# Kernel tuning notes

Measured on AMD Instinct MI355X. Metric: run time of the kernel, lower is better.

The kernel has to match this reference:

```python
import jax, jax.numpy as jnp
import numpy as np

DIM_IN = 1024
DIM_OUT = 1024
NUM_HEADS = 16
HEAD_DIM = DIM_OUT // NUM_HEADS


def setup_inputs() -> dict:
    key = jax.random.key(0)
    k1, k2, k3, k4 = jax.random.split(key, 4)
    X = jax.random.normal(k1, (4, 2048, DIM_IN), dtype=jnp.float32)
    W_qkv = jax.random.normal(k2, (DIM_IN, 3 * DIM_OUT), dtype=jnp.float32) * (DIM_IN ** -0.5)
    W_out = jax.random.normal(k3, (DIM_OUT, DIM_OUT), dtype=jnp.float32) * (DIM_OUT ** -0.5)
    b_out = jax.random.normal(k4, (DIM_OUT,), dtype=jnp.float32) * 0.01
    return {"X": X, "W_qkv": W_qkv, "W_out": W_out, "b_out": b_out}


def reference(X, W_qkv, W_out, b_out):
    B, S, _ = X.shape
    qkv = X @ W_qkv  # [B, S, 3*dim_out]
    qkv = qkv.reshape(B, S, 3, NUM_HEADS, HEAD_DIM).transpose(2, 0, 3, 1, 4)
    q, k, v = qkv[0], qkv[1], qkv[2]  # each [B, H, S, hd]
    scores = jnp.einsum('bhqd,bhkd->bhqk', q, k)  # [B, H, S, S]
    causal = jnp.triu(jnp.ones((S, S), dtype=bool), k=1)
    scores = jnp.where(causal, -jnp.inf, scores)
    attn = jax.nn.softmax(scores * (HEAD_DIM ** -0.5), axis=-1)
    ctx = jnp.einsum('bhqk,bhkd->bhqd', attn, v)  # [B, H, S, hd]
    ctx = ctx.transpose(0, 2, 1, 3).reshape(B, S, DIM_OUT)
    return ctx @ W_out + b_out
```

## Files before the change

### kernel.cpp

```cpp
#include <hip/hip_runtime.h>
#include <hip/hip_bf16.h>

typedef __bf16 bf16_t;
typedef __bf16 bf16x8 __attribute__((ext_vector_type(8)));
typedef __bf16 bf16x4 __attribute__((ext_vector_type(4)));
typedef float f32x4 __attribute__((ext_vector_type(4)));

#define AS1(p) ((const __attribute__((address_space(1))) void*)(p))
#define AS3(p) ((__attribute__((address_space(3))) void*)(p))

#define QSCALE 0.1803368801111204f

__global__ void cast_x_kernel(const float* __restrict__ X, bf16_t* __restrict__ Xb) {
  int i = (blockIdx.x * 256 + threadIdx.x) * 4;
  float4 v = *(const float4*)(X + i);
  bf16x4 o;
  o[0] = (bf16_t)v.x; o[1] = (bf16_t)v.y; o[2] = (bf16_t)v.z; o[3] = (bf16_t)v.w;
  *(bf16x4*)(Xb + i) = o;
}

__global__ void transpose_cast_kernel(const float* __restrict__ W, bf16_t* __restrict__ Wt,
                                      int K, int N) {
  __shared__ float tile[32][33];
  int n0 = blockIdx.x * 32, k0 = blockIdx.y * 32;
  int tx = threadIdx.x, ty = threadIdx.y;
  for (int r = ty; r < 32; r += 8)
    tile[r][tx] = W[(size_t)(k0 + r) * N + n0 + tx];
  __syncthreads();
  for (int r = ty; r < 32; r += 8)
    Wt[(size_t)(n0 + r) * K + k0 + tx] = (bf16_t)tile[tx][r];
}

__global__ __launch_bounds__(256) void gemm_qkv_kernel(
    const bf16_t* __restrict__ A, const bf16_t* __restrict__ Bt,
    bf16_t* __restrict__ Qb, bf16_t* __restrict__ Kb, bf16_t* __restrict__ Vt) {
  __shared__ __align__(16) bf16_t As[128 * 32];
  __shared__ __align__(16) bf16_t Bs[128 * 32];
  const int tid = threadIdx.x;
  const int lane = tid & 63, wave = tid >> 6;
  const int quad = lane >> 4, l15 = lane & 15;
  const int wr = wave >> 1, wc = wave & 1;
  const int m0 = blockIdx.x * 128, n0 = blockIdx.y * 128;
  f32x4 acc[4][4];
  const f32x4 vzero = {0.f, 0.f, 0.f, 0.f};
#pragma unroll
  for (int i = 0; i < 4; i++)
#pragma unroll
    for (int j = 0; j < 4; j++) acc[i][j] = vzero;

  for (int kb = 0; kb < 1024; kb += 32) {
    __syncthreads();
#pragma unroll
    for (int i = 0; i < 2; i++) {
      int c = i * 256 + tid;
      int row = c >> 2, kc = c & 3;
      __builtin_amdgcn_global_load_lds(AS1(A + (size_t)(m0 + row) * 1024 + kb + kc * 8),
                                       AS3(As + c * 8), 16, 0, 0);
    }
#pragma unroll
    for (int i = 0; i < 2; i++) {
      int c = i * 256 + tid;
      int row = c >> 2, kc = c & 3;
      __builtin_amdgcn_global_load_lds(AS1(Bt + (size_t)(n0 + row) * 1024 + kb + kc * 8),
                                       AS3(Bs + c * 8), 16, 0, 0);
    }
    __builtin_amdgcn_s_waitcnt(0);
    __syncthreads();
    bf16x8 af[4], bfr[4];
#pragma unroll
    for (int t = 0; t < 4; t++) {
      af[t]  = *(const bf16x8*)(As + (wr * 64 + t * 16 + l15) * 32 + quad * 8);
      bfr[t] = *(const bf16x8*)(Bs + (wc * 64 + t * 16 + l15) * 32 + quad * 8);
    }
#pragma unroll
    for (int mt = 0; mt < 4; mt++)
#pragma unroll
      for (int nt = 0; nt < 4; nt++)
        acc[mt][nt] = __builtin_amdgcn_mfma_f32_16x16x32_bf16(af[mt], bfr[nt], acc[mt][nt], 0, 0, 0);
  }
#pragma unroll
  for (int nt = 0; nt < 4; nt++) {
    int gn = n0 + wc * 64 + nt * 16 + l15;
    int which = gn >> 10;
    int rem = gn & 1023;
    int hh = rem >> 6, dd = rem & 63;
    if (which == 2) {
#pragma unroll
      for (int mt = 0; mt < 4; mt++) {
        int gm0 = m0 + wr * 64 + mt * 16 + quad * 4;
        int b = gm0 >> 11, s = gm0 & 2047;
        bf16x4 o;
#pragma unroll
        for (int r = 0; r < 4; r++) o[r] = (bf16_t)acc[mt][nt][r];
        *(bf16x4*)(Vt + ((size_t)((b << 4) + hh) * 64 + dd) * 2048 + s) = o;
      }
    } else {
      bf16_t* dst = (which == 0) ? Qb : Kb;
      float scl = (which == 0) ? QSCALE : 1.0f;
#pragma unroll
      for (int mt = 0; mt < 4; mt++) {
#pragma unroll
        for (int r = 0; r < 4; r++) {
          int gm = m0 + wr * 64 + mt * 16 + quad * 4 + r;
          int b = gm >> 11, s = gm & 2047;
          dst[((size_t)((b << 4) + hh) * 2048 + s) * 64 + dd] = (bf16_t)(acc[mt][nt][r] * scl);
        }
      }
    }
  }
}

__global__ __launch_bounds__(256, 3) void attn_kernel(
    const bf16_t* __restrict__ Qg_, const bf16_t* __restrict__ Kg_,
    const bf16_t* __restrict__ Vtg_, bf16_t* __restrict__ ctx) {
  __shared__ __align__(16) bf16_t Ks[128 * 72];
  __shared__ __align__(16) bf16_t Vst[64 * 136];
  __shared__ __align__(16) bf16_t Ps[64 * 128];
  const int tid = threadIdx.x;
  const int lane = tid & 63, w = tid >> 6;
  const int quad = lane >> 4, l15 = lane & 15;

  const int g = blockIdx.x >> 7;
  const int idx = blockIdx.x & 127;
  const int bh = idx >> 1, p = idx & 1;
  const int LENS[6][3] = {{16, 7, 0}, {15, 8, 0}, {14, 6, 2},
                          {13, 5, 4}, {12, 10, 1}, {11, 9, 3}};
  const int ntile = (g < 2) ? 2 : 3;

  const int b = bh >> 4, h = bh & 15;
  const size_t base = (size_t)bh * 2048 * 64;
  const bf16_t* Kg = Kg_ + base;
  const bf16_t* Vtg = Vtg_ + base;

  bf16x8 bone;
#pragma unroll
  for (int e = 0; e < 8; e++) bone[e] = (bf16_t)1.0f;

  bf16x8 kr[4], vr[4];
#pragma unroll
  for (int i = 0; i < 4; i++) {
    int c = i * 256 + tid;
    int r = c >> 3, dc = c & 7;
    kr[i] = *(const bf16x8*)(Kg + (size_t)r * 64 + dc * 8);
  }
#pragma unroll
  for (int i = 0; i < 4; i++) {
    int c = i * 256 + tid;
    int r = c >> 4, cc = c & 15;
    vr[i] = *(const bf16x8*)(Vtg + (size_t)r * 2048 + cc * 8);
  }

  const f32x4 vzero = {0.f, 0.f, 0.f, 0.f};

  for (int ti = 0; ti < ntile; ti++) {
    const int L = LENS[g][ti];
    const int qb = 2 * (L - 1) + p;

    bf16x8 aq[2];
#pragma unroll
    for (int ks = 0; ks < 2; ks++)
      aq[ks] = *(const bf16x8*)(Qg_ + base + (size_t)qb * 64 * 64 +
                                (size_t)(w * 16 + l15) * 64 + ks * 32 + quad * 8);

    f32x4 Oacc[4], Lacc;
#pragma unroll
    for (int dt = 0; dt < 4; dt++) Oacc[dt] = vzero;
    Lacc = vzero;

    for (int j = 0; j < L; j++) {
      __syncthreads();
#pragma unroll
      for (int i = 0; i < 4; i++) {
        int c = i * 256 + tid;
        int r = c >> 3, dc = c & 7;
        *(bf16x8*)(Ks + r * 72 + dc * 8) = kr[i];
      }
#pragma unroll
      for (int i = 0; i < 4; i++) {
        int c = i * 256 + tid;
        int r = c >> 4, cc = c & 15;
        *(bf16x8*)(Vst + r * 136 + cc * 8) = vr[i];
      }
      __syncthreads();

      const bool havenext = (j + 1 < L) || (ti + 1 < ntile);
      if (havenext) {
        const int jn = (j + 1 < L) ? j + 1 : 0;
#pragma unroll
        for (int i = 0; i < 4; i++) {
          int c = i * 256 + tid;
          int r = c >> 3, dc = c & 7;
          kr[i] = *(const bf16x8*)(Kg + ((size_t)jn * 128 + r) * 64 + dc * 8);
        }
#pragma unroll
        for (int i = 0; i < 4; i++) {
          int c = i * 256 + tid;
          int r = c >> 4, cc = c & 15;
          vr[i] = *(const bf16x8*)(Vtg + (size_t)r * 2048 + jn * 128 + cc * 8);
        }
      }

      f32x4 sc[8];
#pragma unroll
      for (int nt = 0; nt < 8; nt++) sc[nt] = vzero;
#pragma unroll
      for (int nt = 0; nt < 8; nt++) {
#pragma unroll
        for (int ks = 0; ks < 2; ks++) {
          bf16x8 bk = *(const bf16x8*)(Ks + (nt * 16 + l15) * 72 + ks * 32 + quad * 8);
          sc[nt] = __builtin_amdgcn_mfma_f32_16x16x32_bf16(aq[ks], bk, sc[nt], 0, 0, 0);
        }
      }

      if (j == L - 1) {
        int kg = j * 128 + l15;
        int qg = qb * 64 + w * 16 + quad * 4;
#pragma unroll
        for (int nt = 0; nt < 8; nt++)
#pragma unroll
          for (int r = 0; r < 4; r++)
            if (kg + nt * 16 > qg + r) sc[nt][r] = -INFINITY;
      }

#pragma unroll
      for (int nt = 0; nt < 8; nt++) {
        int cc = 2 * nt + (l15 >> 3);
        int pc = (cc ^ (quad << 1)) * 8 + (l15 & 7);
#pragma unroll
        for (int r = 0; r < 4; r++) {
          float pp = __builtin_exp2f(sc[nt][r]);
          Ps[(w * 16 + quad * 4 + r) * 128 + pc] = (bf16_t)pp;
        }
      }

#pragma unroll
      for (int ks = 0; ks < 4; ks++) {
        int pcc = ((ks * 4 + quad) ^ ((l15 >> 2) << 1)) * 8;
        bf16x8 ap = *(const bf16x8*)(Ps + (w * 16 + l15) * 128 + pcc);
        Lacc = __builtin_amdgcn_mfma_f32_16x16x32_bf16(ap, bone, Lacc, 0, 0, 0);
#pragma unroll
        for (int dt = 0; dt < 4; dt++) {
          bf16x8 bv = *(const bf16x8*)(Vst + (dt * 16 + l15) * 136 + ks * 32 + quad * 8);
          Oacc[dt] = __builtin_amdgcn_mfma_f32_16x16x32_bf16(ap, bv, Oacc[dt], 0, 0, 0);
        }
      }
    }

    float rl[4];
#pragma unroll
    for (int r = 0; r < 4; r++) rl[r] = __builtin_amdgcn_rcpf(Lacc[r]);
#pragma unroll
    for (int dt = 0; dt < 4; dt++)
#pragma unroll
      for (int r = 0; r < 4; r++) {
        int qg = qb * 64 + w * 16 + quad * 4 + r;
        ctx[((size_t)b * 2048 + qg) * 1024 + h * 64 + dt * 16 + l15] =
            (bf16_t)(Oacc[dt][r] * rl[r]);
      }
  }
}

__global__ __launch_bounds__(256) void gemm_out_kernel(
    const bf16_t* __restrict__ A, const bf16_t* __restrict__ Bt,
    const float* __restrict__ bias, float* __restrict__ out) {
  __shared__ __align__(16) bf16_t As[128 * 32];
  __shared__ __align__(16) bf16_t Bs[128 * 32];
  const int tid = threadIdx.x;
  const int lane = tid & 63, wave = tid >> 6;
  const int quad = lane >> 4, l15 = lane & 15;
  const int wr = wave >> 1, wc = wave & 1;
  const int m0 = blockIdx.x * 128, n0 = blockIdx.y * 128;
  f32x4 acc[4][4];
  const f32x4 vzero = {0.f, 0.f, 0.f, 0.f};
#pragma unroll
  for (int i = 0; i < 4; i++)
#pragma unroll
    for (int j = 0; j < 4; j++) acc[i][j] = vzero;

  for (int kb = 0; kb < 1024; kb += 32) {
    __syncthreads();
#pragma unroll
    for (int i = 0; i < 2; i++) {
      int c = i * 256 + tid;
      int row = c >> 2, kc = c & 3;
      __builtin_amdgcn_global_load_lds(AS1(A + (size_t)(m0 + row) * 1024 + kb + kc * 8),
                                       AS3(As + c * 8), 16, 0, 0);
    }
#pragma unroll
    for (int i = 0; i < 2; i++) {
      int c = i * 256 + tid;
      int row = c >> 2, kc = c & 3;
      __builtin_amdgcn_global_load_lds(AS1(Bt + (size_t)(n0 + row) * 1024 + kb + kc * 8),
                                       AS3(Bs + c * 8), 16, 0, 0);
    }
    __builtin_amdgcn_s_waitcnt(0);
    __syncthreads();
    bf16x8 af[4], bfr[4];
#pragma unroll
    for (int t = 0; t < 4; t++) {
      af[t]  = *(const bf16x8*)(As + (wr * 64 + t * 16 + l15) * 32 + quad * 8);
      bfr[t] = *(const bf16x8*)(Bs + (wc * 64 + t * 16 + l15) * 32 + quad * 8);
    }
#pragma unroll
    for (int mt = 0; mt < 4; mt++)
#pragma unroll
      for (int nt = 0; nt < 4; nt++)
        acc[mt][nt] = __builtin_amdgcn_mfma_f32_16x16x32_bf16(af[mt], bfr[nt], acc[mt][nt], 0, 0, 0);
  }
#pragma unroll
  for (int nt = 0; nt < 4; nt++) {
    int gn = n0 + wc * 64 + nt * 16 + l15;
    float bv = bias[gn];
#pragma unroll
    for (int mt = 0; mt < 4; mt++) {
#pragma unroll
      for (int r = 0; r < 4; r++) {
        int gm = m0 + wr * 64 + mt * 16 + quad * 4 + r;
        out[(size_t)gm * 1024 + gn] = acc[mt][nt][r] + bv;
      }
    }
  }
}

extern "C" void kernel_launch(void* const* d_in, const int* in_sizes, int n_in,
                              void* d_out, int out_size, void* d_ws, size_t ws_size,
                              hipStream_t stream) {
  (void)in_sizes; (void)n_in; (void)out_size; (void)ws_size;
  const float* X     = (const float*)d_in[0];
  const float* W_qkv = (const float*)d_in[1];
  const float* W_out = (const float*)d_in[2];
  const float* b_out = (const float*)d_in[3];
  float* out = (float*)d_out;

  char* ws = (char*)d_ws;
  bf16_t* Xb    = (bf16_t*)(ws);
  bf16_t* Wqkvt = (bf16_t*)(ws + 16777216);
  bf16_t* Woutt = (bf16_t*)(ws + 23068672);
  bf16_t* Qb    = (bf16_t*)(ws + 25165824);
  bf16_t* Kb    = (bf16_t*)(ws + 41943040);
  bf16_t* Vt    = (bf16_t*)(ws + 58720256);
  bf16_t* ctx   = (bf16_t*)(ws + 75497472);

  cast_x_kernel<<<8192, 256, 0, stream>>>(X, Xb);
  transpose_cast_kernel<<<dim3(96, 32), dim3(32, 8), 0, stream>>>(W_qkv, Wqkvt, 1024, 3072);
  transpose_cast_kernel<<<dim3(32, 32), dim3(32, 8), 0, stream>>>(W_out, Woutt, 1024, 1024);
  gemm_qkv_kernel<<<dim3(64, 24), 256, 0, stream>>>(Xb, Wqkvt, Qb, Kb, Vt);
  attn_kernel<<<dim3(768), 256, 0, stream>>>(Qb, Kb, Vt, ctx);
  gemm_out_kernel<<<dim3(64, 8), 256, 0, stream>>>(ctx, Woutt, b_out, out);
}
```

Measured before the change: 273.5 us.

## Enlarge attention query tile to 128 rows with paired causal block scheduling

The attention kernel now processes 128 query rows per tile (32 per wave, two MFMA row tiles) instead of 64. Each K/V block staged in LDS is therefore reused across twice as many queries, halving K/V global loads and LDS staging per query. Load balancing switches from the 6-group LENS table to pairing query block pp with 15-pp, so every workgroup handles 17 KV blocks. The grid drops to 512 workgroups, and the larger P buffer and extra accumulators lower the occupancy bound from 3 to 2 workgroups per CU, which reduces latency hiding.

```diff
diff --git a/kernel.cpp b/kernel.cpp
--- a/kernel.cpp
+++ b/kernel.cpp
@@ -110,23 +110,18 @@
   }
 }
 
-__global__ __launch_bounds__(256, 3) void attn_kernel(
+__global__ __launch_bounds__(256, 2) void attn_kernel(
     const bf16_t* __restrict__ Qg_, const bf16_t* __restrict__ Kg_,
     const bf16_t* __restrict__ Vtg_, bf16_t* __restrict__ ctx) {
   __shared__ __align__(16) bf16_t Ks[128 * 72];
   __shared__ __align__(16) bf16_t Vst[64 * 136];
-  __shared__ __align__(16) bf16_t Ps[64 * 128];
+  __shared__ __align__(16) bf16_t Ps[128 * 128];
   const int tid = threadIdx.x;
   const int lane = tid & 63, w = tid >> 6;
   const int quad = lane >> 4, l15 = lane & 15;
 
-  const int g = blockIdx.x >> 7;
-  const int idx = blockIdx.x & 127;
-  const int bh = idx >> 1, p = idx & 1;
-  const int LENS[6][3] = {{16, 7, 0}, {15, 8, 0}, {14, 6, 2},
-                          {13, 5, 4}, {12, 10, 1}, {11, 9, 3}};
-  const int ntile = (g < 2) ? 2 : 3;
-
+  const int bh = blockIdx.x >> 3;
+  const int pp = blockIdx.x & 7;
   const int b = bh >> 4, h = bh & 15;
   const size_t base = (size_t)bh * 2048 * 64;
   const bf16_t* Kg = Kg_ + base;
@@ -152,20 +147,26 @@
 
   const f32x4 vzero = {0.f, 0.f, 0.f, 0.f};
 
-  for (int ti = 0; ti < ntile; ti++) {
-    const int L = LENS[g][ti];
-    const int qb = 2 * (L - 1) + p;
-
-    bf16x8 aq[2];
-#pragma unroll
-    for (int ks = 0; ks < 2; ks++)
-      aq[ks] = *(const bf16x8*)(Qg_ + base + (size_t)qb * 64 * 64 +
-                                (size_t)(w * 16 + l15) * 64 + ks * 32 + quad * 8);
-
-    f32x4 Oacc[4], Lacc;
-#pragma unroll
-    for (int dt = 0; dt < 4; dt++) Oacc[dt] = vzero;
-    Lacc = vzero;
+  for (int ti = 0; ti < 2; ti++) {
+    const int qb = (ti == 0) ? pp : 15 - pp;
+    const int L = qb + 1;
+
+    bf16x8 aq[2][2];
+#pragma unroll
+    for (int mt = 0; mt < 2; mt++)
+#pragma unroll
+      for (int ks = 0; ks < 2; ks++)
+        aq[mt][ks] = *(const bf16x8*)(Qg_ + base +
+                                      (size_t)(qb * 128 + w * 32 + mt * 16 + l15) * 64 +
+                                      ks * 32 + quad * 8);
+
+    f32x4 Oacc[2][4], Lacc[2];
+#pragma unroll
+    for (int mt = 0; mt < 2; mt++) {
+#pragma unroll
+      for (int dt = 0; dt < 4; dt++) Oacc[mt][dt] = vzero;
+      Lacc[mt] = vzero;
+    }
 
     for (int j = 0; j < L; j++) {
       __syncthreads();
@@ -183,7 +184,7 @@
       }
       __syncthreads();
 
-      const bool havenext = (j + 1 < L) || (ti + 1 < ntile);
+      const bool havenext = (j + 1 < L) || (ti == 0);
       if (havenext) {
         const int jn = (j + 1 < L) ? j + 1 : 0;
 #pragma unroll
@@ -200,63 +201,77 @@
         }
       }
 
-      f32x4 sc[8];
-#pragma unroll
-      for (int nt = 0; nt < 8; nt++) sc[nt] = vzero;
-#pragma unroll
-      for (int nt = 0; nt < 8; nt++) {
-#pragma unroll
-        for (int ks = 0; ks < 2; ks++) {
-          bf16x8 bk = *(const bf16x8*)(Ks + (nt * 16 + l15) * 72 + ks * 32 + quad * 8);
-          sc[nt] = __builtin_amdgcn_mfma_f32_16x16x32_bf16(aq[ks], bk, sc[nt], 0, 0, 0);
-        }
-      }
-
-      if (j == L - 1) {
-        int kg = j * 128 + l15;
-        int qg = qb * 64 + w * 16 + quad * 4;
-#pragma unroll
-        for (int nt = 0; nt < 8; nt++)
-#pragma unroll
-          for (int r = 0; r < 4; r++)
-            if (kg + nt * 16 > qg + r) sc[nt][r] = -INFINITY;
-      }
-
-#pragma unroll
-      for (int nt = 0; nt < 8; nt++) {
-        int cc = 2 * nt + (l15 >> 3);
-        int pc = (cc ^ (quad << 1)) * 8 + (l15 & 7);
-#pragma unroll
-        for (int r = 0; r < 4; r++) {
-          float pp = __builtin_exp2f(sc[nt][r]);
-          Ps[(w * 16 + quad * 4 + r) * 128 + pc] = (bf16_t)pp;
+      const bool diag = (j == L - 1);
+
+#pragma unroll
+      for (int half = 0; half < 2; half++) {
+        f32x4 sch[4][2];
+#pragma unroll
+        for (int nt4 = 0; nt4 < 4; nt4++) {
+          const int nt = half * 4 + nt4;
+          bf16x8 bk0 = *(const bf16x8*)(Ks + (nt * 16 + l15) * 72 + 0 * 32 + quad * 8);
+          bf16x8 bk1 = *(const bf16x8*)(Ks + (nt * 16 + l15) * 72 + 1 * 32 + quad * 8);
+#pragma unroll
+          for (int mt = 0; mt < 2; mt++) {
+            f32x4 s = __builtin_amdgcn_mfma_f32_16x16x32_bf16(aq[mt][0], bk0, vzero, 0, 0, 0);
+            sch[nt4][mt] = __builtin_amdgcn_mfma_f32_16x16x32_bf16(aq[mt][1], bk1, s, 0, 0, 0);
+          }
+        }
+#pragma unroll
+        for (int nt4 = 0; nt4 < 4; nt4++) {
+          const int nt = half * 4 + nt4;
+          const int cc = 2 * nt + (l15 >> 3);
+          const int pc = (cc ^ (quad << 1)) * 8 + (l15 & 7);
+#pragma unroll
+          for (int mt = 0; mt < 2; mt++) {
+            const int prow = w * 32 + mt * 16 + quad * 4;
+#pragma unroll
+            for (int r = 0; r < 4; r++) {
+              float x = sch[nt4][mt][r];
+              if (diag) {
+                int kg = (L - 1) * 128 + nt * 16 + l15;
+                int qg = qb * 128 + prow + r;
+                if (kg > qg) x = -INFINITY;
+              }
+              Ps[(prow + r) * 128 + pc] = (bf16_t)__builtin_exp2f(x);
+            }
+          }
         }
       }
 
 #pragma unroll
       for (int ks = 0; ks < 4; ks++) {
-        int pcc = ((ks * 4 + quad) ^ ((l15 >> 2) << 1)) * 8;
-        bf16x8 ap = *(const bf16x8*)(Ps + (w * 16 + l15) * 128 + pcc);
-        Lacc = __builtin_amdgcn_mfma_f32_16x16x32_bf16(ap, bone, Lacc, 0, 0, 0);
+        const int pcc = ((ks * 4 + quad) ^ ((l15 >> 2) << 1)) * 8;
+        bf16x8 ap[2];
+#pragma unroll
+        for (int mt = 0; mt < 2; mt++) {
+          ap[mt] = *(const bf16x8*)(Ps + (w * 32 + mt * 16 + l15) * 128 + pcc);
+          Lacc[mt] = __builtin_amdgcn_mfma_f32_16x16x32_bf16(ap[mt], bone, Lacc[mt], 0, 0, 0);
+        }
 #pragma unroll
         for (int dt = 0; dt < 4; dt++) {
           bf16x8 bv = *(const bf16x8*)(Vst + (dt * 16 + l15) * 136 + ks * 32 + quad * 8);
-          Oacc[dt] = __builtin_amdgcn_mfma_f32_16x16x32_bf16(ap, bv, Oacc[dt], 0, 0, 0);
-        }
-      }
-    }
-
-    float rl[4];
-#pragma unroll
-    for (int r = 0; r < 4; r++) rl[r] = __builtin_amdgcn_rcpf(Lacc[r]);
-#pragma unroll
-    for (int dt = 0; dt < 4; dt++)
-#pragma unroll
-      for (int r = 0; r < 4; r++) {
-        int qg = qb * 64 + w * 16 + quad * 4 + r;
-        ctx[((size_t)b * 2048 + qg) * 1024 + h * 64 + dt * 16 + l15] =
-            (bf16_t)(Oacc[dt][r] * rl[r]);
-      }
+#pragma unroll
+          for (int mt = 0; mt < 2; mt++)
+            Oacc[mt][dt] = __builtin_amdgcn_mfma_f32_16x16x32_bf16(ap[mt], bv, Oacc[mt][dt], 0, 0, 0);
+        }
+      }
+    }
+
+#pragma unroll
+    for (int mt = 0; mt < 2; mt++) {
+      float rl[4];
+#pragma unroll
+      for (int r = 0; r < 4; r++) rl[r] = __builtin_amdgcn_rcpf(Lacc[mt][r]);
+#pragma unroll
+      for (int dt = 0; dt < 4; dt++)
+#pragma unroll
+        for (int r = 0; r < 4; r++) {
+          int qg = qb * 128 + w * 32 + mt * 16 + quad * 4 + r;
+          ctx[((size_t)b * 2048 + qg) * 1024 + h * 64 + dt * 16 + l15] =
+              (bf16_t)(Oacc[mt][dt][r] * rl[r]);
+        }
+    }
   }
 }
 
@@ -345,6 +360,6 @@
   transpose_cast_kernel<<<dim3(96, 32), dim3(32, 8), 0, stream>>>(W_qkv, Wqkvt, 1024, 3072);
   transpose_cast_kernel<<<dim3(32, 32), dim3(32, 8), 0, stream>>>(W_out, Woutt, 1024, 1024);
   gemm_qkv_kernel<<<dim3(64, 24), 256, 0, stream>>>(Xb, Wqkvt, Qb, Kb, Vt);
-  attn_kernel<<<dim3(768), 256, 0, stream>>>(Qb, Kb, Vt, ctx);
+  attn_kernel<<<dim3(512), 256, 0, stream>>>(Qb, Kb, Vt, ctx);
   gemm_out_kernel<<<dim3(64, 8), 256, 0, stream>>>(ctx, Woutt, b_out, out);
 }
```

Result: no change. 272.8 us (-0.2%).
